# Optimization experiments

Measured on AMD Instinct MI355X. Metric: run time of the kernel, lower is better.

The kernel has to match this reference:

```python
import jax, jax.numpy as jnp
import numpy as np

N = 8192
E = 262144
IN_F = 256
OUT_F = 64
H = 2
SLOPE = 0.2
NEG = -9e15


def _xavier(key, shape, gain):
    fan_in, fan_out = shape[-2], shape[-1]
    a = gain * np.sqrt(6.0 / (fan_in + fan_out))
    return jax.random.uniform(key, shape, jnp.float32, -a, a)


def setup_inputs() -> dict:
    key = jax.random.key(0)
    k_x, k_e, k_w, k_a1, k_a2 = jax.random.split(key, 5)
    gain = np.sqrt(2.0)
    return {
        "x": jax.random.normal(k_x, (N, IN_F), jnp.float32),
        "edge_index": jax.random.randint(k_e, (2, E), 0, N, jnp.int64),
        # per-head params (torch Linear stores weight [out,in]; we store [in,out])
        "W": _xavier(k_w, (H, IN_F, OUT_F), gain),
        "a1": _xavier(k_a1, (H, OUT_F), gain),
        "a2": _xavier(k_a2, (H, OUT_F), gain),
    }


def reference(x, edge_index, W, a1, a2):
    n = x.shape[0]
    # dense adjacency mask from COO edges (to_dense_adj: adj[src, dst] += 1; only adj>0 matters)
    adj = jnp.zeros((n, n), jnp.float32).at[edge_index[0], edge_index[1]].add(1.0)
    mask = adj > 0  # [N, N]

    xh = jnp.einsum('ni,hio->hno', x, W)          # [H, N, out]
    s1 = jnp.einsum('hno,ho->hn', xh, a1)          # a1(x): [H, N]
    s2 = jnp.einsum('hno,ho->hn', xh, a2)          # a2(x): [H, N]
    e = jnp.where(mask[None], s1[:, :, None] + s2[:, None, :], NEG)  # [H, N, N]
    e = jnp.where(e >= 0, e, SLOPE * e)            # leaky_relu
    att = jax.nn.softmax(e, axis=-1)               # [H, N, N]
    out = jnp.einsum('hnm,hmo->hno', att, xh)      # [H, N, out]
    # concat heads along feature dim (is_final_layer=False)
    return jnp.transpose(out, (1, 0, 2)).reshape(n, H * OUT_F)
```

## Files before the change

### kernel.cpp

```cpp
#include <hip/hip_runtime.h>

#define NN    8192
#define INF_  256
#define OUTF  64
#define NH    2
#define NE    262144
#define NW    256
#define SLOPE 0.2f

typedef __attribute__((ext_vector_type(8))) short short8;
typedef __attribute__((ext_vector_type(4))) float f32x4;

__device__ __forceinline__ unsigned short f2bf(float f) {
  unsigned int u = __float_as_uint(f);
  u += 0x7fffu + ((u >> 16) & 1u);
  return (unsigned short)(u >> 16);
}
__device__ __forceinline__ float bf2f(unsigned short u) {
  return __uint_as_float(((unsigned int)u) << 16);
}

__global__ __launch_bounds__(256) void gemm_kernel(
    const float* __restrict__ x, const float* __restrict__ W,
    const float* __restrict__ a1, const float* __restrict__ a2,
    unsigned short* __restrict__ xhb, float2* __restrict__ s1v,
    float2* __restrict__ s2v, unsigned* __restrict__ bits) {
  const int b = blockIdx.x, t = threadIdx.x;

  {
    uint4* bp = (uint4*)(bits + (size_t)b * 4096) + t;
    const uint4 z = {0u, 0u, 0u, 0u};
    bp[0] = z; bp[256] = z; bp[512] = z; bp[768] = z;
  }

  const int l = t & 63, w = t >> 6;
  const int lo = l & 15, hi = l >> 4;
  const int n0 = b * 16;
  __shared__ float p1s[4][16], p2s[4][16];

  const int tc0 = w * 2, tc1 = w * 2 + 1;
  const int h0 = tc0 >> 2, h1 = tc1 >> 2;
  const int col0 = (tc0 * 16 + lo) & 63, col1 = (tc1 * 16 + lo) & 63;
  const float* wp0 = W + (size_t)h0 * (INF_ * OUTF) + (size_t)(hi * 8) * OUTF + col0;
  const float* wp1 = W + (size_t)h1 * (INF_ * OUTF) + (size_t)(hi * 8) * OUTF + col1;
  const float* xp = x + (size_t)(n0 + lo) * INF_ + hi * 8;

  f32x4 acc0 = {0.f, 0.f, 0.f, 0.f};
  f32x4 acc1 = {0.f, 0.f, 0.f, 0.f};

#define KSTEP(ks)                                                              \
  {                                                                            \
    const float4 f0 = *(const float4*)(xp + (ks) * 32);                        \
    const float4 f1 = *(const float4*)(xp + (ks) * 32 + 4);                    \
    short8 a_;                                                                 \
    a_[0] = (short)f2bf(f0.x); a_[1] = (short)f2bf(f0.y);                      \
    a_[2] = (short)f2bf(f0.z); a_[3] = (short)f2bf(f0.w);                      \
    a_[4] = (short)f2bf(f1.x); a_[5] = (short)f2bf(f1.y);                      \
    a_[6] = (short)f2bf(f1.z); a_[7] = (short)f2bf(f1.w);                      \
    const float* wq0 = wp0 + (size_t)(ks) * 32 * OUTF;                         \
    short8 b0_;                                                                \
    b0_[0] = (short)f2bf(wq0[0 * OUTF]); b0_[1] = (short)f2bf(wq0[1 * OUTF]);  \
    b0_[2] = (short)f2bf(wq0[2 * OUTF]); b0_[3] = (short)f2bf(wq0[3 * OUTF]);  \
    b0_[4] = (short)f2bf(wq0[4 * OUTF]); b0_[5] = (short)f2bf(wq0[5 * OUTF]);  \
    b0_[6] = (short)f2bf(wq0[6 * OUTF]); b0_[7] = (short)f2bf(wq0[7 * OUTF]);  \
    acc0 = __builtin_amdgcn_mfma_f32_16x16x32_bf16(a_, b0_, acc0, 0, 0, 0);    \
    const float* wq1 = wp1 + (size_t)(ks) * 32 * OUTF;                         \
    short8 b1_;                                                                \
    b1_[0] = (short)f2bf(wq1[0 * OUTF]); b1_[1] = (short)f2bf(wq1[1 * OUTF]);  \
    b1_[2] = (short)f2bf(wq1[2 * OUTF]); b1_[3] = (short)f2bf(wq1[3 * OUTF]);  \
    b1_[4] = (short)f2bf(wq1[4 * OUTF]); b1_[5] = (short)f2bf(wq1[5 * OUTF]);  \
    b1_[6] = (short)f2bf(wq1[6 * OUTF]); b1_[7] = (short)f2bf(wq1[7 * OUTF]);  \
    acc1 = __builtin_amdgcn_mfma_f32_16x16x32_bf16(a_, b1_, acc1, 0, 0, 0);    \
  }

  KSTEP(0) KSTEP(1) KSTEP(2) KSTEP(3) KSTEP(4) KSTEP(5) KSTEP(6) KSTEP(7)
#undef KSTEP

  {
    unsigned short* o0 = xhb + ((size_t)h0 * NN + n0 + hi * 4) * OUTF + col0;
    unsigned short* o1 = xhb + ((size_t)h1 * NN + n0 + hi * 4) * OUTF + col1;
    o0[0 * OUTF] = f2bf(acc0[0]); o0[1 * OUTF] = f2bf(acc0[1]);
    o0[2 * OUTF] = f2bf(acc0[2]); o0[3 * OUTF] = f2bf(acc0[3]);
    o1[0 * OUTF] = f2bf(acc1[0]); o1[1 * OUTF] = f2bf(acc1[1]);
    o1[2 * OUTF] = f2bf(acc1[2]); o1[3 * OUTF] = f2bf(acc1[3]);
  }
  const float a10 = a1[h0 * OUTF + col0], a11 = a1[h1 * OUTF + col1];
  const float a20 = a2[h0 * OUTF + col0], a21 = a2[h1 * OUTF + col1];
#pragma unroll
  for (int r = 0; r < 4; ++r) {
    float p1v = acc0[r] * a10 + acc1[r] * a11;
    float p2v = acc0[r] * a20 + acc1[r] * a21;
#pragma unroll
    for (int s = 1; s < 16; s <<= 1) {
      p1v += __shfl_xor(p1v, s, 64);
      p2v += __shfl_xor(p2v, s, 64);
    }
    if (lo == 0) {
      p1s[w][hi * 4 + r] = p1v;
      p2s[w][hi * 4 + r] = p2v;
    }
  }
  __syncthreads();
  if (t < 16) {
    float2 v1, v2;
    v1.x = p1s[0][t] + p1s[1][t];  v1.y = p1s[2][t] + p1s[3][t];
    v2.x = p2s[0][t] + p2s[1][t];  v2.y = p2s[2][t] + p2s[3][t];
    s1v[n0 + t] = v1;
    s2v[n0 + t] = v2;
  }
}

__global__ __launch_bounds__(256) void edge_kernel(const int* __restrict__ ei,
                                                   unsigned* __restrict__ bits) {
  const int e = blockIdx.x * 256 + threadIdx.x;
  __shared__ int s_nz;
  if (threadIdx.x == 0) s_nz = 0;
  __syncthreads();
  if (((const unsigned int*)ei)[2 * e + 1] != 0u) s_nz = 1;
  __syncthreads();
  int i, j;
  if (s_nz == 0) {
    i = (int)((const long long*)ei)[e];
    j = (int)((const long long*)ei)[NE + e];
  } else {
    i = ei[e];
    j = ei[NE + e];
  }
  atomicOr(&bits[(size_t)i * NW + (j >> 5)], 1u << (j & 31));
}

__global__ __launch_bounds__(128) void agg_kernel(const unsigned short* __restrict__ xhb,
                                                  const float2* __restrict__ s1v,
                                                  const float2* __restrict__ s2v,
                                                  const unsigned* __restrict__ bits,
                                                  float* __restrict__ out) {
  const int i = blockIdx.x;
  const int t = threadIdx.x;
  const int h = t >> 6, lane = t & 63;
  __shared__ int   cjs[NH][256];
  __shared__ float wts[NH][256];

  const uint4 bv = *(const uint4*)(bits + (size_t)i * NW + lane * 4);
  const int myc = __popc(bv.x) + __popc(bv.y) + __popc(bv.z) + __popc(bv.w);
  int incl = myc;
#pragma unroll
  for (int s = 1; s < 64; s <<= 1) {
    const int v = __shfl_up(incl, s, 64);
    if (lane >= s) incl += v;
  }
  int pos = incl - myc;
  const int dt = __shfl(incl, 63, 64);
  const int d = __builtin_amdgcn_readfirstlane(dt > 256 ? 256 : dt);
  {
    unsigned wv; int bj;
    wv = bv.x; bj = lane * 128;
    while (wv) { const int bb = __ffs(wv) - 1; if (pos < 256) cjs[h][pos] = bj + bb; ++pos; wv &= wv - 1; }
    wv = bv.y; bj = lane * 128 + 32;
    while (wv) { const int bb = __ffs(wv) - 1; if (pos < 256) cjs[h][pos] = bj + bb; ++pos; wv &= wv - 1; }
    wv = bv.z; bj = lane * 128 + 64;
    while (wv) { const int bb = __ffs(wv) - 1; if (pos < 256) cjs[h][pos] = bj + bb; ++pos; wv &= wv - 1; }
    wv = bv.w; bj = lane * 128 + 96;
    while (wv) { const int bb = __ffs(wv) - 1; if (pos < 256) cjs[h][pos] = bj + bb; ++pos; wv &= wv - 1; }
  }
  __syncthreads();

  const unsigned short* base = xhb + (size_t)h * NN * OUTF;
  const int r8 = lane >> 3, c8 = lane & 7;
  float accv[8] = {0.f, 0.f, 0.f, 0.f, 0.f, 0.f, 0.f, 0.f};
  float inv;

  if (d == 0) {
    for (int p = r8; p < NN; p += 8) {
      const short8 v = *(const short8*)(base + (size_t)p * OUTF + c8 * 8);
#pragma unroll
      for (int m = 0; m < 8; ++m) accv[m] += bf2f((unsigned short)v[m]);
    }
    inv = 1.f / (float)NN;
  } else if (d <= 64) {
    const bool kp = lane < d;
    const int j = kp ? cjs[h][lane] : 0;
    float sc = -1e30f;
    if (kp) {
      const float2 s1i2 = s1v[i];
      const float2 s2j2 = s2v[j];
      sc = (h ? s1i2.y : s1i2.x) + (h ? s2j2.y : s2j2.x);
      sc = (sc >= 0.f) ? sc : SLOPE * sc;
    }
    float m = sc;
#pragma unroll
    for (int s = 32; s > 0; s >>= 1) m = fmaxf(m, __shfl_xor(m, s, 64));
    const float wt = kp ? __expf(sc - m) : 0.f;
    float ds = wt;
#pragma unroll
    for (int s = 32; s > 0; s >>= 1) ds += __shfl_xor(ds, s, 64);
    inv = 1.f / ds;
#pragma unroll 2
    for (int p = 0; p < d; p += 8) {
      const int pr = p + r8;
      float ww = __shfl(wt, pr, 64);
      int   jj = __shfl(j,  pr, 64);
      ww = (pr < d) ? ww : 0.f;
      jj = (ww > 0.f) ? jj : 0;
      const short8 v = *(const short8*)(base + (size_t)jj * OUTF + c8 * 8);
#pragma unroll
      for (int m2 = 0; m2 < 8; ++m2) accv[m2] += ww * bf2f((unsigned short)v[m2]);
    }
  } else {
    const float2 s1i2 = s1v[i];
    const float s1i = h ? s1i2.y : s1i2.x;
    float m = -1e30f;
    for (int p = lane; p < d; p += 64) {
      const float2 s2j2 = s2v[cjs[h][p]];
      float sc = s1i + (h ? s2j2.y : s2j2.x);
      sc = (sc >= 0.f) ? sc : SLOPE * sc;
      wts[h][p] = sc;
      m = fmaxf(m, sc);
    }
#pragma unroll
    for (int s = 32; s > 0; s >>= 1) m = fmaxf(m, __shfl_xor(m, s, 64));
    float ds = 0.f;
    for (int p = lane; p < d; p += 64) {
      const float w2 = __expf(wts[h][p] - m);
      wts[h][p] = w2;
      ds += w2;
    }
#pragma unroll
    for (int s = 32; s > 0; s >>= 1) ds += __shfl_xor(ds, s, 64);
    inv = 1.f / ds;
#pragma unroll 2
    for (int p = 0; p < d; p += 8) {
      const int pr = p + r8;
      const bool ok = pr < d;
      const float ww = ok ? wts[h][pr] : 0.f;
      const int   jj = ok ? cjs[h][pr] : 0;
      const short8 v = *(const short8*)(base + (size_t)jj * OUTF + c8 * 8);
#pragma unroll
      for (int m2 = 0; m2 < 8; ++m2) accv[m2] += ww * bf2f((unsigned short)v[m2]);
    }
  }

#pragma unroll
  for (int m2 = 0; m2 < 8; ++m2) {
    accv[m2] += __shfl_xor(accv[m2], 8, 64);
    accv[m2] += __shfl_xor(accv[m2], 16, 64);
    accv[m2] += __shfl_xor(accv[m2], 32, 64);
  }
  if (lane < 8) {
    float4 o0, o1;
    o0.x = accv[0] * inv; o0.y = accv[1] * inv;
    o0.z = accv[2] * inv; o0.w = accv[3] * inv;
    o1.x = accv[4] * inv; o1.y = accv[5] * inv;
    o1.z = accv[6] * inv; o1.w = accv[7] * inv;
    float* op = out + (size_t)i * (NH * OUTF) + h * OUTF + lane * 8;
    *(float4*)op = o0;
    *(float4*)(op + 4) = o1;
  }
}

extern "C" void kernel_launch(void* const* d_in, const int* in_sizes, int n_in,
                              void* d_out, int out_size, void* d_ws, size_t ws_size,
                              hipStream_t stream) {
  const float* x  = (const float*)d_in[0];
  const int*   ei = (const int*)d_in[1];
  const float* W  = (const float*)d_in[2];
  const float* a1 = (const float*)d_in[3];
  const float* a2 = (const float*)d_in[4];
  float* out = (float*)d_out;

  char* ws = (char*)d_ws;
  unsigned*       bits = (unsigned*)(ws);
  unsigned short* xhb  = (unsigned short*)(ws + (8u << 20));
  float2*         s1v  = (float2*)(ws + (10u << 20));
  float2*         s2v  = (float2*)(ws + (10u << 20) + (64u << 10));

  gemm_kernel<<<512, 256, 0, stream>>>(x, W, a1, a2, xhb, s1v, s2v, bits);
  edge_kernel<<<NE / 256, 256, 0, stream>>>(ei, bits);
  agg_kernel<<<NN, 128, 0, stream>>>(xhb, s1v, s2v, bits, out);
}
```

Baseline: 43.79 us.

## Fuse edge scatter and aggregation into one persistent kernel with grid barrier

The edge-bitmap scatter and attention aggregation kernels are merged into a single 1024-block kernel separated by a software grid barrier built on agent-scope atomics, and the barrier counter is reset inside the GEMM kernel. Each block now handles eight rows, two per iteration, across two 128-thread halves. This removes one kernel launch and its gap, and gives aggregation fewer, fatter blocks. In exchange the barrier is only safe if all 1024 blocks are co-resident (launch_bounds 256,4 suggests that is assumed), and adds barrier latency plus a __syncthreads per row pair.

```diff
diff --git a/kernel.cpp b/kernel.cpp
--- a/kernel.cpp
+++ b/kernel.cpp
@@ -7,6 +7,7 @@
 #define NE    262144
 #define NW    256
 #define SLOPE 0.2f
+#define NBLK2 1024
 
 typedef __attribute__((ext_vector_type(8))) short short8;
 typedef __attribute__((ext_vector_type(4))) float f32x4;
@@ -20,11 +21,29 @@
   return __uint_as_float(((unsigned int)u) << 16);
 }
 
+__device__ __forceinline__ void grid_barrier(unsigned* bar, int nblk) {
+  __syncthreads();
+  if (threadIdx.x == 0) {
+    __threadfence();
+    const unsigned arrived =
+        __hip_atomic_fetch_add(&bar[0], 1u, __ATOMIC_ACQ_REL, __HIP_MEMORY_SCOPE_AGENT) + 1u;
+    if (arrived == (unsigned)nblk) {
+      __hip_atomic_store(&bar[1], 1u, __ATOMIC_RELEASE, __HIP_MEMORY_SCOPE_AGENT);
+    } else {
+      while (__hip_atomic_load(&bar[1], __ATOMIC_ACQUIRE, __HIP_MEMORY_SCOPE_AGENT) == 0u)
+        __builtin_amdgcn_s_sleep(2);
+    }
+    __threadfence();
+  }
+  __syncthreads();
+}
+
 __global__ __launch_bounds__(256) void gemm_kernel(
     const float* __restrict__ x, const float* __restrict__ W,
     const float* __restrict__ a1, const float* __restrict__ a2,
     unsigned short* __restrict__ xhb, float2* __restrict__ s1v,
-    float2* __restrict__ s2v, unsigned* __restrict__ bits) {
+    float2* __restrict__ s2v, unsigned* __restrict__ bits,
+    unsigned* __restrict__ bar) {
   const int b = blockIdx.x, t = threadIdx.x;
 
   {
@@ -32,6 +51,7 @@
     const uint4 z = {0u, 0u, 0u, 0u};
     bp[0] = z; bp[256] = z; bp[512] = z; bp[768] = z;
   }
+  if (b == 0 && t < 2) bar[t] = 0u;
 
   const int l = t & 63, w = t >> 6;
   const int lo = l & 15, hi = l >> 4;
@@ -110,150 +130,157 @@
   }
 }
 
-__global__ __launch_bounds__(256) void edge_kernel(const int* __restrict__ ei,
-                                                   unsigned* __restrict__ bits) {
-  const int e = blockIdx.x * 256 + threadIdx.x;
-  __shared__ int s_nz;
-  if (threadIdx.x == 0) s_nz = 0;
-  __syncthreads();
-  if (((const unsigned int*)ei)[2 * e + 1] != 0u) s_nz = 1;
-  __syncthreads();
-  int i, j;
-  if (s_nz == 0) {
-    i = (int)((const long long*)ei)[e];
-    j = (int)((const long long*)ei)[NE + e];
-  } else {
-    i = ei[e];
-    j = ei[NE + e];
-  }
-  atomicOr(&bits[(size_t)i * NW + (j >> 5)], 1u << (j & 31));
-}
-
-__global__ __launch_bounds__(128) void agg_kernel(const unsigned short* __restrict__ xhb,
-                                                  const float2* __restrict__ s1v,
-                                                  const float2* __restrict__ s2v,
-                                                  const unsigned* __restrict__ bits,
-                                                  float* __restrict__ out) {
-  const int i = blockIdx.x;
-  const int t = threadIdx.x;
-  const int h = t >> 6, lane = t & 63;
-  __shared__ int   cjs[NH][256];
-  __shared__ float wts[NH][256];
-
-  const uint4 bv = *(const uint4*)(bits + (size_t)i * NW + lane * 4);
-  const int myc = __popc(bv.x) + __popc(bv.y) + __popc(bv.z) + __popc(bv.w);
-  int incl = myc;
-#pragma unroll
-  for (int s = 1; s < 64; s <<= 1) {
-    const int v = __shfl_up(incl, s, 64);
-    if (lane >= s) incl += v;
-  }
-  int pos = incl - myc;
-  const int dt = __shfl(incl, 63, 64);
-  const int d = __builtin_amdgcn_readfirstlane(dt > 256 ? 256 : dt);
+__global__ __launch_bounds__(256, 4) void edge_agg_kernel(
+    const int* __restrict__ ei, const unsigned short* __restrict__ xhb,
+    const float2* __restrict__ s1v, const float2* __restrict__ s2v,
+    unsigned* __restrict__ bits, unsigned* __restrict__ bar,
+    float* __restrict__ out) {
+  const int b = blockIdx.x, t = threadIdx.x;
+
   {
-    unsigned wv; int bj;
-    wv = bv.x; bj = lane * 128;
-    while (wv) { const int bb = __ffs(wv) - 1; if (pos < 256) cjs[h][pos] = bj + bb; ++pos; wv &= wv - 1; }
-    wv = bv.y; bj = lane * 128 + 32;
-    while (wv) { const int bb = __ffs(wv) - 1; if (pos < 256) cjs[h][pos] = bj + bb; ++pos; wv &= wv - 1; }
-    wv = bv.z; bj = lane * 128 + 64;
-    while (wv) { const int bb = __ffs(wv) - 1; if (pos < 256) cjs[h][pos] = bj + bb; ++pos; wv &= wv - 1; }
-    wv = bv.w; bj = lane * 128 + 96;
-    while (wv) { const int bb = __ffs(wv) - 1; if (pos < 256) cjs[h][pos] = bj + bb; ++pos; wv &= wv - 1; }
-  }
-  __syncthreads();
-
+    __shared__ int s_nz;
+    if (t == 0) s_nz = 0;
+    __syncthreads();
+    const int e = b * 256 + t;
+    if (((const unsigned int*)ei)[2 * e + 1] != 0u) s_nz = 1;
+    __syncthreads();
+    int i_, j_;
+    if (s_nz == 0) {
+      i_ = (int)((const long long*)ei)[e];
+      j_ = (int)((const long long*)ei)[NE + e];
+    } else {
+      i_ = ei[e];
+      j_ = ei[NE + e];
+    }
+    atomicOr(&bits[(size_t)i_ * NW + (j_ >> 5)], 1u << (j_ & 31));
+  }
+
+  grid_barrier(bar, NBLK2);
+
+  __shared__ int   cjs[2][256];
+  __shared__ float wts[2][NH][256];
+  __shared__ int   sdeg[2];
+  const int sub = t >> 7, th = t & 127, h = th >> 6, lane = th & 63;
   const unsigned short* base = xhb + (size_t)h * NN * OUTF;
   const int r8 = lane >> 3, c8 = lane & 7;
-  float accv[8] = {0.f, 0.f, 0.f, 0.f, 0.f, 0.f, 0.f, 0.f};
-  float inv;
-
-  if (d == 0) {
-    for (int p = r8; p < NN; p += 8) {
-      const short8 v = *(const short8*)(base + (size_t)p * OUTF + c8 * 8);
-#pragma unroll
-      for (int m = 0; m < 8; ++m) accv[m] += bf2f((unsigned short)v[m]);
-    }
-    inv = 1.f / (float)NN;
-  } else if (d <= 64) {
-    const bool kp = lane < d;
-    const int j = kp ? cjs[h][lane] : 0;
-    float sc = -1e30f;
-    if (kp) {
+
+  for (int it = 0; it < 4; ++it) {
+    const int i = b * 8 + it * 2 + sub;
+
+    if (h == 0) {
+      const uint4 bv = *(const uint4*)(bits + (size_t)i * NW + lane * 4);
+      const int myc = __popc(bv.x) + __popc(bv.y) + __popc(bv.z) + __popc(bv.w);
+      int incl = myc;
+#pragma unroll
+      for (int s = 1; s < 64; s <<= 1) {
+        const int v = __shfl_up(incl, s, 64);
+        if (lane >= s) incl += v;
+      }
+      int pos = incl - myc;
+      if (lane == 63) sdeg[sub] = (incl > 256) ? 256 : incl;
+      unsigned wv; int bj;
+      wv = bv.x; bj = lane * 128;
+      while (wv) { const int bb = __ffs(wv) - 1; if (pos < 256) cjs[sub][pos] = bj + bb; ++pos; wv &= wv - 1; }
+      wv = bv.y; bj = lane * 128 + 32;
+      while (wv) { const int bb = __ffs(wv) - 1; if (pos < 256) cjs[sub][pos] = bj + bb; ++pos; wv &= wv - 1; }
+      wv = bv.z; bj = lane * 128 + 64;
+      while (wv) { const int bb = __ffs(wv) - 1; if (pos < 256) cjs[sub][pos] = bj + bb; ++pos; wv &= wv - 1; }
+      wv = bv.w; bj = lane * 128 + 96;
+      while (wv) { const int bb = __ffs(wv) - 1; if (pos < 256) cjs[sub][pos] = bj + bb; ++pos; wv &= wv - 1; }
+    }
+    __syncthreads();
+    const int d = sdeg[sub];
+
+    float accv[8] = {0.f, 0.f, 0.f, 0.f, 0.f, 0.f, 0.f, 0.f};
+    float inv;
+
+    if (d == 0) {
+      for (int p = r8; p < NN; p += 8) {
+        const short8 v = *(const short8*)(base + (size_t)p * OUTF + c8 * 8);
+#pragma unroll
+        for (int m = 0; m < 8; ++m) accv[m] += bf2f((unsigned short)v[m]);
+      }
+      inv = 1.f / (float)NN;
+    } else if (d <= 64) {
+      const bool kp = lane < d;
+      const int j = kp ? cjs[sub][lane] : 0;
+      float sc = -1e30f;
+      if (kp) {
+        const float2 s1i2 = s1v[i];
+        const float2 s2j2 = s2v[j];
+        sc = (h ? s1i2.y : s1i2.x) + (h ? s2j2.y : s2j2.x);
+        sc = (sc >= 0.f) ? sc : SLOPE * sc;
+      }
+      float m = sc;
+#pragma unroll
+      for (int s = 32; s > 0; s >>= 1) m = fmaxf(m, __shfl_xor(m, s, 64));
+      const float wt = kp ? __expf(sc - m) : 0.f;
+      float ds = wt;
+#pragma unroll
+      for (int s = 32; s > 0; s >>= 1) ds += __shfl_xor(ds, s, 64);
+      inv = 1.f / ds;
+#pragma unroll 2
+      for (int p = 0; p < d; p += 8) {
+        const int pr = p + r8;
+        float ww = __shfl(wt, pr, 64);
+        int   jj = __shfl(j,  pr, 64);
+        ww = (pr < d) ? ww : 0.f;
+        jj = (ww > 0.f) ? jj : 0;
+        const short8 v = *(const short8*)(base + (size_t)jj * OUTF + c8 * 8);
+#pragma unroll
+        for (int m2 = 0; m2 < 8; ++m2) accv[m2] += ww * bf2f((unsigned short)v[m2]);
+      }
+    } else {
       const float2 s1i2 = s1v[i];
-      const float2 s2j2 = s2v[j];
-      sc = (h ? s1i2.y : s1i2.x) + (h ? s2j2.y : s2j2.x);
-      sc = (sc >= 0.f) ? sc : SLOPE * sc;
-    }
-    float m = sc;
-#pragma unroll
-    for (int s = 32; s > 0; s >>= 1) m = fmaxf(m, __shfl_xor(m, s, 64));
-    const float wt = kp ? __expf(sc - m) : 0.f;
-    float ds = wt;
-#pragma unroll
-    for (int s = 32; s > 0; s >>= 1) ds += __shfl_xor(ds, s, 64);
-    inv = 1.f / ds;
+      const float s1i = h ? s1i2.y : s1i2.x;
+      float m = -1e30f;
+      for (int p = lane; p < d; p += 64) {
+        const float2 s2j2 = s2v[cjs[sub][p]];
+        float sc = s1i + (h ? s2j2.y : s2j2.x);
+        sc = (sc >= 0.f) ? sc : SLOPE * sc;
+        wts[sub][h][p] = sc;
+        m = fmaxf(m, sc);
+      }
+#pragma unroll
+      for (int s = 32; s > 0; s >>= 1) m = fmaxf(m, __shfl_xor(m, s, 64));
+      float ds = 0.f;
+      for (int p = lane; p < d; p += 64) {
+        const float w2 = __expf(wts[sub][h][p] - m);
+        wts[sub][h][p] = w2;
+        ds += w2;
+      }
+#pragma unroll
+      for (int s = 32; s > 0; s >>= 1) ds += __shfl_xor(ds, s, 64);
+      inv = 1.f / ds;
 #pragma unroll 2
-    for (int p = 0; p < d; p += 8) {
-      const int pr = p + r8;
-      float ww = __shfl(wt, pr, 64);
-      int   jj = __shfl(j,  pr, 64);
-      ww = (pr < d) ? ww : 0.f;
-      jj = (ww > 0.f) ? jj : 0;
-      const short8 v = *(const short8*)(base + (size_t)jj * OUTF + c8 * 8);
-#pragma unroll
-      for (int m2 = 0; m2 < 8; ++m2) accv[m2] += ww * bf2f((unsigned short)v[m2]);
-    }
-  } else {
-    const float2 s1i2 = s1v[i];
-    const float s1i = h ? s1i2.y : s1i2.x;
-    float m = -1e30f;
-    for (int p = lane; p < d; p += 64) {
-      const float2 s2j2 = s2v[cjs[h][p]];
-      float sc = s1i + (h ? s2j2.y : s2j2.x);
-      sc = (sc >= 0.f) ? sc : SLOPE * sc;
-      wts[h][p] = sc;
-      m = fmaxf(m, sc);
-    }
-#pragma unroll
-    for (int s = 32; s > 0; s >>= 1) m = fmaxf(m, __shfl_xor(m, s, 64));
-    float ds = 0.f;
-    for (int p = lane; p < d; p += 64) {
-      const float w2 = __expf(wts[h][p] - m);
-      wts[h][p] = w2;
-      ds += w2;
-    }
-#pragma unroll
-    for (int s = 32; s > 0; s >>= 1) ds += __shfl_xor(ds, s, 64);
-    inv = 1.f / ds;
-#pragma unroll 2
-    for (int p = 0; p < d; p += 8) {
-      const int pr = p + r8;
-      const bool ok = pr < d;
-      const float ww = ok ? wts[h][pr] : 0.f;
-      const int   jj = ok ? cjs[h][pr] : 0;
-      const short8 v = *(const short8*)(base + (size_t)jj * OUTF + c8 * 8);
-#pragma unroll
-      for (int m2 = 0; m2 < 8; ++m2) accv[m2] += ww * bf2f((unsigned short)v[m2]);
-    }
-  }
-
-#pragma unroll
-  for (int m2 = 0; m2 < 8; ++m2) {
-    accv[m2] += __shfl_xor(accv[m2], 8, 64);
-    accv[m2] += __shfl_xor(accv[m2], 16, 64);
-    accv[m2] += __shfl_xor(accv[m2], 32, 64);
-  }
-  if (lane < 8) {
-    float4 o0, o1;
-    o0.x = accv[0] * inv; o0.y = accv[1] * inv;
-    o0.z = accv[2] * inv; o0.w = accv[3] * inv;
-    o1.x = accv[4] * inv; o1.y = accv[5] * inv;
-    o1.z = accv[6] * inv; o1.w = accv[7] * inv;
-    float* op = out + (size_t)i * (NH * OUTF) + h * OUTF + lane * 8;
-    *(float4*)op = o0;
-    *(float4*)(op + 4) = o1;
+      for (int p = 0; p < d; p += 8) {
+        const int pr = p + r8;
+        const bool ok = pr < d;
+        const float ww = ok ? wts[sub][h][pr] : 0.f;
+        const int   jj = ok ? cjs[sub][pr] : 0;
+        const short8 v = *(const short8*)(base + (size_t)jj * OUTF + c8 * 8);
+#pragma unroll
+        for (int m2 = 0; m2 < 8; ++m2) accv[m2] += ww * bf2f((unsigned short)v[m2]);
+      }
+    }
+
+#pragma unroll
+    for (int m2 = 0; m2 < 8; ++m2) {
+      accv[m2] += __shfl_xor(accv[m2], 8, 64);
+      accv[m2] += __shfl_xor(accv[m2], 16, 64);
+      accv[m2] += __shfl_xor(accv[m2], 32, 64);
+    }
+    if (lane < 8) {
+      float4 o0, o1;
+      o0.x = accv[0] * inv; o0.y = accv[1] * inv;
+      o0.z = accv[2] * inv; o0.w = accv[3] * inv;
+      o1.x = accv[4] * inv; o1.y = accv[5] * inv;
+      o1.z = accv[6] * inv; o1.w = accv[7] * inv;
+      float* op = out + (size_t)i * (NH * OUTF) + h * OUTF + lane * 8;
+      *(float4*)op = o0;
+      *(float4*)(op + 4) = o1;
+    }
+    __syncthreads();
   }
 }
 
@@ -272,8 +299,8 @@
   unsigned short* xhb  = (unsigned short*)(ws + (8u << 20));
   float2*         s1v  = (float2*)(ws + (10u << 20));
   float2*         s2v  = (float2*)(ws + (10u << 20) + (64u << 10));
-
-  gemm_kernel<<<512, 256, 0, stream>>>(x, W, a1, a2, xhb, s1v, s2v, bits);
-  edge_kernel<<<NE / 256, 256, 0, stream>>>(ei, bits);
-  agg_kernel<<<NN, 128, 0, stream>>>(xhb, s1v, s2v, bits, out);
-}
+  unsigned*       bar  = (unsigned*)(ws + (11u << 20));
+
+  gemm_kernel<<<512, 256, 0, stream>>>(x, W, a1, a2, xhb, s1v, s2v, bits, bar);
+  edge_agg_kernel<<<NBLK2, 256, 0, stream>>>(ei, xhb, s1v, s2v, bits, bar, out);
+}
```

New measurement: 124.8 us. 185% more time.
